# Optimization experiments

Measured on AMD Instinct MI355X. Metric: run time of the kernel, lower is better.

## Reference

```python
import jax, jax.numpy as jnp
import numpy as np

NEG_SLOPE = 0.2


def setup_inputs() -> dict:
    key = jax.random.key(0)
    ks = jax.random.split(key, 12)
    N, D = 50000, 256
    H, C = 4, 128          # heads, per-head channels; H*C = gnn_hidden_dim = 512
    E = 800000
    edge_index = jax.random.randint(ks[0], (2, E), 0, N, dtype=jnp.int64)
    edge_weight = jax.random.uniform(ks[1], (E,), dtype=jnp.float32)
    s = 1.0 / np.sqrt(D)
    return {
        'edge_index': edge_index,
        'edge_weight': edge_weight,
        'emb':     jax.random.normal(ks[2], (N, D), jnp.float32),
        'W':       jax.random.normal(ks[3], (D, H * C), jnp.float32) * s,
        'att_src': jax.random.normal(ks[4], (H, C), jnp.float32) * s,
        'att_dst': jax.random.normal(ks[5], (H, C), jnp.float32) * s,
        'att_edge': jax.random.normal(ks[6], (H, C), jnp.float32) * s,
        'W_edge':  jax.random.normal(ks[7], (1, H * C), jnp.float32),
        'bias':    jnp.zeros((H * C,), jnp.float32),
        'W_out':   jax.random.normal(ks[8], (H * C, D), jnp.float32) * s,
        'b_out':   jnp.zeros((D,), jnp.float32),
    }


def reference(edge_index, edge_weight, emb, W, att_src, att_dst, att_edge,
              W_edge, bias, W_out, b_out):
    N, D = emb.shape
    H, C = att_src.shape
    src, dst = edge_index[0], edge_index[1]
    E = src.shape[0]

    # GATConv: shared linear projection for src and dst (in_channels is int)
    x = (emb @ W).reshape(N, H, C)                     # [N,H,C]

    # add self loops; edge_attr for loops = per-dst mean of incoming edge_attr
    ones = jnp.ones((E,), emb.dtype)
    cnt = jax.ops.segment_sum(ones, dst, num_segments=N)
    ea_mean = jax.ops.segment_sum(edge_weight, dst, num_segments=N) / jnp.maximum(cnt, 1.0)
    loop = jnp.arange(N, dtype=src.dtype)
    src_f = jnp.concatenate([src, loop])
    dst_f = jnp.concatenate([dst, loop])
    ea = jnp.concatenate([edge_weight, ea_mean])[:, None]   # [E+N, 1]

    e_feat = (ea @ W_edge).reshape(-1, H, C)            # [E+N,H,C]

    a_src = jnp.einsum('nhc,hc->nh', x, att_src)        # [N,H]
    a_dst = jnp.einsum('nhc,hc->nh', x, att_dst)
    a_e = jnp.einsum('ehc,hc->eh', e_feat, att_edge)    # [E+N,H]

    alpha = jax.nn.leaky_relu(a_src[src_f] + a_dst[dst_f] + a_e, NEG_SLOPE)
    # segment softmax over destination neighborhoods
    m = jax.ops.segment_max(alpha, dst_f, num_segments=N)
    alpha = jnp.exp(alpha - m[dst_f])
    denom = jax.ops.segment_sum(alpha, dst_f, num_segments=N)
    alpha = alpha / (denom[dst_f] + 1e-16)              # [E+N,H]

    msg = x[src_f] * alpha[..., None]                   # [E+N,H,C]
    out = jax.ops.segment_sum(msg, dst_f, num_segments=N).reshape(N, H * C) + bias

    return out @ W_out + b_out                          # [N,D]
```

## Files before the change

### kernel.cpp

```cpp
#include <hip/hip_runtime.h>
#include <cstdint>
#include <cstddef>

#define NEG_SLOPE 0.2f
#define HC 512
#define NH 4
#define CAP 64

typedef __attribute__((ext_vector_type(8))) short bf16x8;
typedef __attribute__((ext_vector_type(4))) float f32x4;

__device__ inline float lrelu(float z) { return z > 0.f ? z : NEG_SLOPE * z; }

__device__ inline unsigned short f2bf(float f) {
    unsigned u = __float_as_uint(f);
    u += 0x7FFFu + ((u >> 16) & 1u);
    return (unsigned short)(u >> 16);
}
__device__ inline float bflo(unsigned v) { return __uint_as_float(v << 16); }
__device__ inline float bfhi(unsigned v) { return __uint_as_float(v & 0xffff0000u); }

#define GLOAD16(gp, lp) \
    __builtin_amdgcn_global_load_lds( \
        (const __attribute__((address_space(1))) unsigned int*)(const void*)(gp), \
        (__attribute__((address_space(3))) unsigned int*)(void*)(lp), 16, 0, 0)

__global__ __launch_bounds__(256) void mega1_kernel(
        const int* __restrict__ ei, const float* __restrict__ ew, int E,
        int* __restrict__ cnt, int2* __restrict__ csr2,
        const float* __restrict__ W, const float* __restrict__ W_out,
        const float* __restrict__ att_s, const float* __restrict__ att_d,
        const float* __restrict__ W_edge, const float* __restrict__ att_edge,
        const float* __restrict__ bias, const float* __restrict__ b_out,
        unsigned short* __restrict__ Wb, unsigned short* __restrict__ WoT,
        float* __restrict__ watt, float* __restrict__ bc4, float* __restrict__ sh,
        const float4* __restrict__ embf4, uint2* __restrict__ embq,
        int nQuads, int nCast) {
    int b = blockIdx.x, t = threadIdx.x;
    int r6 = b % 6, q6 = b / 6;

    if (r6 == 0) {
        int lane = t & 63;
        unsigned long long nzm = __ballot(ei[2 * lane + 1] != 0);
        int is64 = (nzm == 0ull) ? 1 : 0;
        int base = q6 * 1024;

        int dv[4], sv[4];
        float wv[4];
        bool ok[4];
        #pragma unroll
        for (int r = 0; r < 4; ++r) {
            int e = base + r * 256 + t;
            ok[r] = (e < E);
            if (ok[r]) {
                size_t de = (size_t)E + e;
                dv[r] = is64 ? ei[2 * de] : ei[de];
                sv[r] = is64 ? ei[2 * (size_t)e] : ei[e];
                wv[r] = ew[e];
            }
        }
        int pos[4];
        #pragma unroll
        for (int r = 0; r < 4; ++r)
            if (ok[r]) pos[r] = atomicAdd(&cnt[dv[r]], 1);
        #pragma unroll
        for (int r = 0; r < 4; ++r)
            if (ok[r] && pos[r] < CAP)
                csr2[(size_t)dv[r] * CAP + pos[r]] =
                    make_int2(sv[r], __float_as_int(wv[r]));
        return;
    }

    int aux = q6 * 5 + r6 - 1;
    if (aux < 128) {
        int i = aux * 256 + t;
        float4 v = reinterpret_cast<const float4*>(W)[i];
        ushort4 o;
        o.x = f2bf(v.x); o.y = f2bf(v.y); o.z = f2bf(v.z); o.w = f2bf(v.w);
        reinterpret_cast<ushort4*>(Wb)[i] = o;
    } else if (aux < 640) {
        int idx = (aux - 128) * 256 + t;
        int r = idx >> 8, c = idx & 255;
        WoT[(size_t)c * 512 + r] = f2bf(W_out[idx]);
    } else if (aux < 648) {
        int i = aux - 640;
        int h = i & 3;
        const float* att = (i < 4) ? att_s : att_d;
        float s = 0.f;
        for (int c = 0; c < 128; ++c)
            s += W[(size_t)t * HC + h * 128 + c] * att[h * 128 + c];
        watt[i * 256 + t] = s;
    } else if (aux < 652) {
        int part = aux - 648;
        int j0 = part * 128;
        float s = (part == 0) ? b_out[t] : 0.f;
        for (int j = j0; j < j0 + 128; ++j)
            s += bias[j] * W_out[(size_t)j * 256 + t];
        bc4[part * 256 + t] = s;
    } else if (aux == 652) {
        if (t < NH) {
            float s = 0.f;
            for (int c = 0; c < 128; ++c)
                s += W_edge[t * 128 + c] * att_edge[t * 128 + c];
            sh[t] = s;
        }
    } else if (aux < 653 + nCast) {
        int base = (aux - 653) * 1024;
        #pragma unroll
        for (int j = 0; j < 4; ++j) {
            int i = base + j * 256 + t;
            if (i < nQuads) {
                float4 v = embf4[i];
                uint2 o;
                o.x = (unsigned)f2bf(v.x) | ((unsigned)f2bf(v.y) << 16);
                o.y = (unsigned)f2bf(v.z) | ((unsigned)f2bf(v.w) << 16);
                embq[i] = o;
            }
        }
    }
}

__global__ __launch_bounds__(256) void mega2_kernel(
        const unsigned short* __restrict__ WoT, const unsigned short* __restrict__ Wb,
        unsigned short* __restrict__ MT,
        const uint2* __restrict__ embq, const float* __restrict__ watt,
        float* __restrict__ a_src, float* __restrict__ a_dst, int N) {
    __shared__ __align__(16) char smem[32768];
    int b = blockIdx.x, t = threadIdx.x;

    if (b < 16) {
        unsigned short* As = (unsigned short*)smem;
        unsigned short* Bs = (unsigned short*)(smem + 16384);
        int lane = t & 63, w = t >> 6;
        int bn = (b & 1) * 128, bm = ((b >> 1) & 1) * 128, z = b >> 2;
        const unsigned short* A  = WoT + (size_t)z * 128;
        const unsigned short* BT = Wb  + (size_t)z * 128;
        int wr = w >> 1, wc = w & 1;

        f32x4 acc[4][4];
        #pragma unroll
        for (int i = 0; i < 4; ++i)
            #pragma unroll
            for (int j = 0; j < 4; ++j)
                acc[i][j] = (f32x4){0.f, 0.f, 0.f, 0.f};

        int lr = lane & 15, kb = lane >> 4;
        int q = lane & 7;

        for (int k0 = 0; k0 < 128; k0 += 64) {
            #pragma unroll
            for (int p = 0; p < 4; ++p) {
                int row = p * 32 + w * 8 + (lane >> 3);
                int ce  = ((q ^ (row & 7)) << 3) + k0;
                int ob  = p * 4096 + w * 1024;
                GLOAD16(A  + (size_t)(bm + row) * 512 + ce, (char*)As + ob);
                GLOAD16(BT + (size_t)(bn + row) * 512 + ce, (char*)Bs + ob);
            }
            __syncthreads();
            #pragma unroll
            for (int kk = 0; kk < 2; ++kk) {
                bf16x8 a[4], bfr[4];
                #pragma unroll
                for (int i = 0; i < 4; ++i) {
                    int row = wr * 64 + i * 16 + lr;
                    a[i] = *reinterpret_cast<const bf16x8*>(
                        &As[row * 64 + (((kk * 4 + kb) ^ (row & 7)) << 3)]);
                }
                #pragma unroll
                for (int j = 0; j < 4; ++j) {
                    int row = wc * 64 + j * 16 + lr;
                    bfr[j] = *reinterpret_cast<const bf16x8*>(
                        &Bs[row * 64 + (((kk * 4 + kb) ^ (row & 7)) << 3)]);
                }
                #pragma unroll
                for (int i = 0; i < 4; ++i)
                    #pragma unroll
                    for (int j = 0; j < 4; ++j)
                        acc[i][j] = __builtin_amdgcn_mfma_f32_16x16x32_bf16(a[i], bfr[j], acc[i][j], 0, 0, 0);
            }
            __syncthreads();
        }
        int rg = lane >> 4;
        #pragma unroll
        for (int i = 0; i < 4; ++i)
            #pragma unroll
            for (int r = 0; r < 4; ++r) {
                int row = bm + wr * 64 + i * 16 + rg * 4 + r;
                #pragma unroll
                for (int j = 0; j < 4; ++j) {
                    int col = bn + wc * 64 + j * 16 + lr;
                    MT[(size_t)row * 1024 + z * 256 + col] = f2bf(acc[i][j][r]);
                }
            }
    } else {
        int bb = b - 16;
        int wid = t >> 6, lane = t & 63;
        #pragma unroll
        for (int j = 0; j < 4; ++j) {
            int n = bb * 16 + wid * 4 + j;
            if (n >= N) break;
            uint2 v = embq[(size_t)n * 64 + lane];
            float d0 = bflo(v.x), d1 = bfhi(v.x), d2 = bflo(v.y), d3 = bfhi(v.y);
            float r[8];
            #pragma unroll
            for (int i = 0; i < 8; ++i) {
                float4 wv = reinterpret_cast<const float4*>(watt)[i * 64 + lane];
                r[i] = d0 * wv.x + d1 * wv.y + d2 * wv.z + d3 * wv.w;
            }
            #pragma unroll
            for (int off = 32; off > 0; off >>= 1) {
                #pragma unroll
                for (int i = 0; i < 8; ++i) r[i] += __shfl_xor(r[i], off);
            }
            if (lane == 0) {
                size_t bofs = (size_t)n * 4;
                a_src[bofs + 0] = r[0]; a_src[bofs + 1] = r[1];
                a_src[bofs + 2] = r[2]; a_src[bofs + 3] = r[3];
                a_dst[bofs + 0] = r[4]; a_dst[bofs + 1] = r[5];
                a_dst[bofs + 2] = r[6]; a_dst[bofs + 3] = r[7];
            }
        }
    }
}

#define EFMA(W_, V_) { \
    float e0_ = bflo(V_.x), e1_ = bfhi(V_.x), e2_ = bflo(V_.y), e3_ = bfhi(V_.y); \
    a00 += W_.x * e0_; a01 += W_.x * e1_; a02 += W_.x * e2_; a03 += W_.x * e3_; \
    a10 += W_.y * e0_; a11 += W_.y * e1_; a12 += W_.y * e2_; a13 += W_.y * e3_; \
    a20 += W_.z * e0_; a21 += W_.z * e1_; a22 += W_.z * e2_; a23 += W_.z * e3_; \
    a30 += W_.w * e0_; a31 += W_.w * e1_; a32 += W_.w * e2_; a33 += W_.w * e3_; \
    den0 += W_.x; den1 += W_.y; den2 += W_.z; den3 += W_.w; }

__global__ __launch_bounds__(256) void agg_kernel(
        const uint2* __restrict__ embq, const float* __restrict__ a_src,
        const float* __restrict__ a_dst, const int* __restrict__ cnt,
        const float* __restrict__ sh, const int2* __restrict__ csr2,
        uint2* __restrict__ aggn, int N) {
    int wid = threadIdx.x >> 6, lane = threadIdx.x & 63;
    int n = blockIdx.x * 4 + wid;
    if (n >= N) return;
    int deg = cnt[n];
    int m = deg < CAP ? deg : CAP;

    __shared__ int s_src[4][64];
    __shared__ __align__(16) float s_alpha[4][64][4];

    int k1 = 0x7FFFFFFF, k2 = 0x7FFFFFFF;
    if (lane < m) {
        int2 p = csr2[(size_t)n * CAP + lane];
        k1 = p.x; k2 = p.y;
    }
    #pragma unroll
    for (int k = 2; k <= 64; k <<= 1) {
        #pragma unroll
        for (int j = k >> 1; j > 0; j >>= 1) {
            int o1 = __shfl_xor(k1, j);
            int o2 = __shfl_xor(k2, j);
            bool lower = (lane & j) == 0;
            bool asc = (lane & k) == 0;
            bool cmp = (k1 > o1) || (k1 == o1 && k2 > o2);
            if ((cmp == lower) == asc) { k1 = o1; k2 = o2; }
        }
    }
    float wgt = (lane < m) ? __int_as_float(k2) : 0.f;

    float wsl = wgt;
    #pragma unroll
    for (int o = 32; o > 0; o >>= 1) wsl += __shfl_xor(wsl, o);
    float eam = wsl / fmaxf((float)deg, 1.f);

    float ad0 = a_dst[(size_t)n * 4 + 0], ad1 = a_dst[(size_t)n * 4 + 1];
    float ad2 = a_dst[(size_t)n * 4 + 2], ad3 = a_dst[(size_t)n * 4 + 3];
    float sh0 = sh[0], sh1 = sh[1], sh2 = sh[2], sh3 = sh[3];
    float es0 = __expf(lrelu(a_src[(size_t)n * 4 + 0] + ad0 + eam * sh0));
    float es1 = __expf(lrelu(a_src[(size_t)n * 4 + 1] + ad1 + eam * sh1));
    float es2 = __expf(lrelu(a_src[(size_t)n * 4 + 2] + ad2 + eam * sh2));
    float es3 = __expf(lrelu(a_src[(size_t)n * 4 + 3] + ad3 + eam * sh3));

    uint2 xv = embq[(size_t)n * 64 + lane];
    float d0 = bflo(xv.x), d1 = bfhi(xv.x), d2 = bflo(xv.y), d3 = bfhi(xv.y);

    float a00 = es0 * d0, a01 = es0 * d1, a02 = es0 * d2, a03 = es0 * d3;
    float a10 = es1 * d0, a11 = es1 * d1, a12 = es1 * d2, a13 = es1 * d3;
    float a20 = es2 * d0, a21 = es2 * d1, a22 = es2 * d2, a23 = es2 * d3;
    float a30 = es3 * d0, a31 = es3 * d1, a32 = es3 * d2, a33 = es3 * d3;
    float den0 = es0, den1 = es1, den2 = es2, den3 = es3;

    if (lane < m) {
        int s = k1;
        s_src[wid][lane] = s;
        float4 as4 = *reinterpret_cast<const float4*>(&a_src[(size_t)s * 4]);
        s_alpha[wid][lane][0] = __expf(lrelu(as4.x + ad0 + wgt * sh0));
        s_alpha[wid][lane][1] = __expf(lrelu(as4.y + ad1 + wgt * sh1));
        s_alpha[wid][lane][2] = __expf(lrelu(as4.z + ad2 + wgt * sh2));
        s_alpha[wid][lane][3] = __expf(lrelu(as4.w + ad3 + wgt * sh3));
    }
    int e2 = 0;
    for (; e2 + 2 <= m; e2 += 2) {
        int s0 = s_src[wid][e2], s1 = s_src[wid][e2 + 1];
        float4 w0 = *reinterpret_cast<const float4*>(s_alpha[wid][e2]);
        float4 w1 = *reinterpret_cast<const float4*>(s_alpha[wid][e2 + 1]);
        uint2 v0 = embq[(size_t)s0 * 64 + lane];
        uint2 v1 = embq[(size_t)s1 * 64 + lane];
        EFMA(w0, v0); EFMA(w1, v1);
    }
    if (e2 < m) {
        int s0 = s_src[wid][e2];
        float4 w0 = *reinterpret_cast<const float4*>(s_alpha[wid][e2]);
        uint2 v0 = embq[(size_t)s0 * 64 + lane];
        EFMA(w0, v0);
    }

    float i0 = 1.f / (den0 + 1e-16f), i1 = 1.f / (den1 + 1e-16f);
    float i2 = 1.f / (den2 + 1e-16f), i3 = 1.f / (den3 + 1e-16f);
    size_t base = (size_t)n * 256 + lane;
    uint2 o;
    o.x = (unsigned)f2bf(a00 * i0) | ((unsigned)f2bf(a01 * i0) << 16);
    o.y = (unsigned)f2bf(a02 * i0) | ((unsigned)f2bf(a03 * i0) << 16);
    aggn[base] = o;
    o.x = (unsigned)f2bf(a10 * i1) | ((unsigned)f2bf(a11 * i1) << 16);
    o.y = (unsigned)f2bf(a12 * i1) | ((unsigned)f2bf(a13 * i1) << 16);
    aggn[base + 64] = o;
    o.x = (unsigned)f2bf(a20 * i2) | ((unsigned)f2bf(a21 * i2) << 16);
    o.y = (unsigned)f2bf(a22 * i2) | ((unsigned)f2bf(a23 * i2) << 16);
    aggn[base + 128] = o;
    o.x = (unsigned)f2bf(a30 * i3) | ((unsigned)f2bf(a31 * i3) << 16);
    o.y = (unsigned)f2bf(a32 * i3) | ((unsigned)f2bf(a33 * i3) << 16);
    aggn[base + 192] = o;
}

__global__ __launch_bounds__(512) void gemm_out_kernel(
        const unsigned short* __restrict__ A,
        const unsigned short* __restrict__ BT,
        const float* __restrict__ bc4, float* __restrict__ C, int M) {
    __shared__ __align__(16) unsigned short As[128 * 64];
    __shared__ __align__(16) unsigned short Bs[256 * 64];
    int tid = threadIdx.x;
    int lane = tid & 63, w = tid >> 6;
    int bm = blockIdx.x * 128;
    int wr = w >> 2, wc = w & 3;

    f32x4 acc[4][4];
    #pragma unroll
    for (int i = 0; i < 4; ++i)
        #pragma unroll
        for (int j = 0; j < 4; ++j)
            acc[i][j] = (f32x4){0.f, 0.f, 0.f, 0.f};

    int lr = lane & 15, kb = lane >> 4;
    int q = lane & 7;

    for (int k0 = 0; k0 < 1024; k0 += 64) {
        #pragma unroll
        for (int p = 0; p < 2; ++p) {
            int row = p * 64 + w * 8 + (lane >> 3);
            int ce  = ((q ^ (row & 7)) << 3) + k0;
            int ob  = p * 8192 + w * 1024;
            int gr = bm + row; if (gr >= M) gr = M - 1;
            GLOAD16(A + (size_t)gr * 1024 + ce, (char*)As + ob);
        }
        #pragma unroll
        for (int p = 0; p < 4; ++p) {
            int row = p * 64 + w * 8 + (lane >> 3);
            int ce  = ((q ^ (row & 7)) << 3) + k0;
            int ob  = p * 8192 + w * 1024;
            GLOAD16(BT + (size_t)row * 1024 + ce, (char*)Bs + ob);
        }
        __syncthreads();

        #pragma unroll
        for (int kk = 0; kk < 2; ++kk) {
            bf16x8 a[4], b[4];
            #pragma unroll
            for (int i = 0; i < 4; ++i) {
                int row = wr * 64 + i * 16 + lr;
                a[i] = *reinterpret_cast<const bf16x8*>(
                    &As[row * 64 + (((kk * 4 + kb) ^ (row & 7)) << 3)]);
            }
            #pragma unroll
            for (int j = 0; j < 4; ++j) {
                int row = wc * 64 + j * 16 + lr;
                b[j] = *reinterpret_cast<const bf16x8*>(
                    &Bs[row * 64 + (((kk * 4 + kb) ^ (row & 7)) << 3)]);
            }
            #pragma unroll
            for (int i = 0; i < 4; ++i)
                #pragma unroll
                for (int j = 0; j < 4; ++j)
                    acc[i][j] = __builtin_amdgcn_mfma_f32_16x16x32_bf16(a[i], b[j], acc[i][j], 0, 0, 0);
        }
        __syncthreads();
    }

    int rg = lane >> 4;
    #pragma unroll
    for (int i = 0; i < 4; ++i) {
        #pragma unroll
        for (int r = 0; r < 4; ++r) {
            int row = bm + wr * 64 + i * 16 + rg * 4 + r;
            if (row >= M) continue;
            #pragma unroll
            for (int j = 0; j < 4; ++j) {
                int col = wc * 64 + j * 16 + lr;
                float bval = bc4[col] + bc4[256 + col] + bc4[512 + col] + bc4[768 + col];
                C[(size_t)row * 256 + col] = acc[i][j][r] + bval;
            }
        }
    }
}

extern "C" void kernel_launch(void* const* d_in, const int* in_sizes, int n_in,
                              void* d_out, int out_size, void* d_ws, size_t ws_size,
                              hipStream_t stream) {
    const int*   edge_index  = (const int*)d_in[0];
    const float* edge_weight = (const float*)d_in[1];
    const float* emb         = (const float*)d_in[2];
    const float* W           = (const float*)d_in[3];
    const float* att_src     = (const float*)d_in[4];
    const float* att_dst     = (const float*)d_in[5];
    const float* att_edge    = (const float*)d_in[6];
    const float* W_edge      = (const float*)d_in[7];
    const float* bias        = (const float*)d_in[8];
    const float* W_out       = (const float*)d_in[9];
    const float* b_out       = (const float*)d_in[10];
    float* out = (float*)d_out;

    const int E = in_sizes[1];
    const int D = 256;
    const int N = in_sizes[2] / D;
    const int mb = (N + 127) / 128;
    const int nEmb = (N + 15) / 16;
    const int nEdge4 = (E + 1023) / 1024;
    const int nQuads = N * 64;
    const int nCast = (nQuads + 1023) / 1024;

    char* ws = (char*)d_ws;
    size_t off = 0;
    auto alloc = [&](size_t bytes) {
        size_t o = off;
        off += (bytes + 255) & ~(size_t)255;
        return o;
    };
    unsigned short* embb  = (unsigned short*)(ws + alloc((size_t)N * D * 2));
    unsigned short* aggn  = (unsigned short*)(ws + alloc((size_t)N * 1024 * 2));
    unsigned short* Wb    = (unsigned short*)(ws + alloc((size_t)D * HC * 2));
    unsigned short* WoT   = (unsigned short*)(ws + alloc((size_t)HC * D * 2));
    unsigned short* MT    = (unsigned short*)(ws + alloc((size_t)256 * 1024 * 2));
    float* watt    = (float*)(ws + alloc(2048 * 4));
    float* bc4     = (float*)(ws + alloc(1024 * 4));
    float* a_src   = (float*)(ws + alloc((size_t)N * 4 * 4));
    float* a_dst   = (float*)(ws + alloc((size_t)N * 4 * 4));
    float* sh      = (float*)(ws + alloc(64));
    size_t zbytes  = (size_t)N * 4;
    size_t zoff    = alloc(zbytes);
    int*   cnt     = (int*)(ws + zoff);
    int2*  csr2    = (int2*)(ws + alloc((size_t)N * CAP * 8));
    (void)ws_size; (void)n_in; (void)out_size;

    hipMemsetAsync(ws + zoff, 0, zbytes, stream);

    mega1_kernel<<<nEdge4 * 6, 256, 0, stream>>>(
        edge_index, edge_weight, E, cnt, csr2,
        W, W_out, att_src, att_dst, W_edge, att_edge, bias, b_out,
        Wb, WoT, watt, bc4, sh,
        (const float4*)emb, (uint2*)embb, nQuads, nCast);

    mega2_kernel<<<16 + nEmb, 256, 0, stream>>>(
        WoT, Wb, MT, (const uint2*)embb, watt, a_src, a_dst, N);

    agg_kernel<<<(N + 3) / 4, 256, 0, stream>>>(
        (const uint2*)embb, a_src, a_dst, cnt, sh, csr2, (uint2*)aggn, N);

    gemm_out_kernel<<<mb, 512, 0, stream>>>(aggn, MT, bc4, out, N);
}
```

Baseline: 231.3 us.

## Fuse emb cast with attention-score projection and split small precompute kernel

Measured after the change: 226.0 us, median of 2. 2.3% less time.

```diff
diff --git a/kernel.cpp b/kernel.cpp
--- a/kernel.cpp
+++ b/kernel.cpp
@@ -25,17 +25,49 @@
         (const __attribute__((address_space(1))) unsigned int*)(const void*)(gp), \
         (__attribute__((address_space(3))) unsigned int*)(void*)(lp), 16, 0, 0)
 
+__global__ __launch_bounds__(256) void prep00_kernel(
+        const float* __restrict__ W, const float* __restrict__ W_out,
+        const float* __restrict__ att_s, const float* __restrict__ att_d,
+        const float* __restrict__ W_edge, const float* __restrict__ att_edge,
+        const float* __restrict__ bias, const float* __restrict__ b_out,
+        float* __restrict__ watt, float* __restrict__ bc4, float* __restrict__ sh,
+        uint4* __restrict__ zptr, int zcount) {
+    int b = blockIdx.x, t = threadIdx.x;
+    if (b < 8) {
+        int h = b & 3;
+        const float* att = (b < 4) ? att_s : att_d;
+        float s = 0.f;
+        for (int c = 0; c < 128; ++c)
+            s += W[(size_t)t * HC + h * 128 + c] * att[h * 128 + c];
+        watt[b * 256 + t] = s;
+    } else if (b < 12) {
+        int part = b - 8;
+        int j0 = part * 128;
+        float s = (part == 0) ? b_out[t] : 0.f;
+        for (int j = j0; j < j0 + 128; ++j)
+            s += bias[j] * W_out[(size_t)j * 256 + t];
+        bc4[part * 256 + t] = s;
+    } else if (b == 12) {
+        if (t < NH) {
+            float s = 0.f;
+            for (int c = 0; c < 128; ++c)
+                s += W_edge[t * 128 + c] * att_edge[t * 128 + c];
+            sh[t] = s;
+        }
+    } else {
+        int idx = (b - 13) * 256 + t;
+        if (idx < zcount) zptr[idx] = (uint4){0u, 0u, 0u, 0u};
+    }
+}
+
 __global__ __launch_bounds__(256) void mega1_kernel(
         const int* __restrict__ ei, const float* __restrict__ ew, int E,
         int* __restrict__ cnt, int2* __restrict__ csr2,
         const float* __restrict__ W, const float* __restrict__ W_out,
-        const float* __restrict__ att_s, const float* __restrict__ att_d,
-        const float* __restrict__ W_edge, const float* __restrict__ att_edge,
-        const float* __restrict__ bias, const float* __restrict__ b_out,
         unsigned short* __restrict__ Wb, unsigned short* __restrict__ WoT,
-        float* __restrict__ watt, float* __restrict__ bc4, float* __restrict__ sh,
-        const float4* __restrict__ embf4, uint2* __restrict__ embq,
-        int nQuads, int nCast) {
+        const float4* __restrict__ embf4, const float* __restrict__ watt,
+        uint2* __restrict__ embq, float* __restrict__ a_src,
+        float* __restrict__ a_dst, int N, int nEmb) {
     int b = blockIdx.x, t = threadIdx.x;
     int r6 = b % 6, q6 = b / 6;
 
@@ -82,130 +114,23 @@
         int idx = (aux - 128) * 256 + t;
         int r = idx >> 8, c = idx & 255;
         WoT[(size_t)c * 512 + r] = f2bf(W_out[idx]);
-    } else if (aux < 648) {
-        int i = aux - 640;
-        int h = i & 3;
-        const float* att = (i < 4) ? att_s : att_d;
-        float s = 0.f;
-        for (int c = 0; c < 128; ++c)
-            s += W[(size_t)t * HC + h * 128 + c] * att[h * 128 + c];
-        watt[i * 256 + t] = s;
-    } else if (aux < 652) {
-        int part = aux - 648;
-        int j0 = part * 128;
-        float s = (part == 0) ? b_out[t] : 0.f;
-        for (int j = j0; j < j0 + 128; ++j)
-            s += bias[j] * W_out[(size_t)j * 256 + t];
-        bc4[part * 256 + t] = s;
-    } else if (aux == 652) {
-        if (t < NH) {
-            float s = 0.f;
-            for (int c = 0; c < 128; ++c)
-                s += W_edge[t * 128 + c] * att_edge[t * 128 + c];
-            sh[t] = s;
-        }
-    } else if (aux < 653 + nCast) {
-        int base = (aux - 653) * 1024;
-        #pragma unroll
-        for (int j = 0; j < 4; ++j) {
-            int i = base + j * 256 + t;
-            if (i < nQuads) {
-                float4 v = embf4[i];
-                uint2 o;
-                o.x = (unsigned)f2bf(v.x) | ((unsigned)f2bf(v.y) << 16);
-                o.y = (unsigned)f2bf(v.z) | ((unsigned)f2bf(v.w) << 16);
-                embq[i] = o;
-            }
-        }
-    }
-}
-
-__global__ __launch_bounds__(256) void mega2_kernel(
-        const unsigned short* __restrict__ WoT, const unsigned short* __restrict__ Wb,
-        unsigned short* __restrict__ MT,
-        const uint2* __restrict__ embq, const float* __restrict__ watt,
-        float* __restrict__ a_src, float* __restrict__ a_dst, int N) {
-    __shared__ __align__(16) char smem[32768];
-    int b = blockIdx.x, t = threadIdx.x;
-
-    if (b < 16) {
-        unsigned short* As = (unsigned short*)smem;
-        unsigned short* Bs = (unsigned short*)(smem + 16384);
-        int lane = t & 63, w = t >> 6;
-        int bn = (b & 1) * 128, bm = ((b >> 1) & 1) * 128, z = b >> 2;
-        const unsigned short* A  = WoT + (size_t)z * 128;
-        const unsigned short* BT = Wb  + (size_t)z * 128;
-        int wr = w >> 1, wc = w & 1;
-
-        f32x4 acc[4][4];
-        #pragma unroll
-        for (int i = 0; i < 4; ++i)
-            #pragma unroll
-            for (int j = 0; j < 4; ++j)
-                acc[i][j] = (f32x4){0.f, 0.f, 0.f, 0.f};
-
-        int lr = lane & 15, kb = lane >> 4;
-        int q = lane & 7;
-
-        for (int k0 = 0; k0 < 128; k0 += 64) {
-            #pragma unroll
-            for (int p = 0; p < 4; ++p) {
-                int row = p * 32 + w * 8 + (lane >> 3);
-                int ce  = ((q ^ (row & 7)) << 3) + k0;
-                int ob  = p * 4096 + w * 1024;
-                GLOAD16(A  + (size_t)(bm + row) * 512 + ce, (char*)As + ob);
-                GLOAD16(BT + (size_t)(bn + row) * 512 + ce, (char*)Bs + ob);
-            }
-            __syncthreads();
-            #pragma unroll
-            for (int kk = 0; kk < 2; ++kk) {
-                bf16x8 a[4], bfr[4];
-                #pragma unroll
-                for (int i = 0; i < 4; ++i) {
-                    int row = wr * 64 + i * 16 + lr;
-                    a[i] = *reinterpret_cast<const bf16x8*>(
-                        &As[row * 64 + (((kk * 4 + kb) ^ (row & 7)) << 3)]);
-                }
-                #pragma unroll
-                for (int j = 0; j < 4; ++j) {
-                    int row = wc * 64 + j * 16 + lr;
-                    bfr[j] = *reinterpret_cast<const bf16x8*>(
-                        &Bs[row * 64 + (((kk * 4 + kb) ^ (row & 7)) << 3)]);
-                }
-                #pragma unroll
-                for (int i = 0; i < 4; ++i)
-                    #pragma unroll
-                    for (int j = 0; j < 4; ++j)
-                        acc[i][j] = __builtin_amdgcn_mfma_f32_16x16x32_bf16(a[i], bfr[j], acc[i][j], 0, 0, 0);
-            }
-            __syncthreads();
-        }
-        int rg = lane >> 4;
-        #pragma unroll
-        for (int i = 0; i < 4; ++i)
-            #pragma unroll
-            for (int r = 0; r < 4; ++r) {
-                int row = bm + wr * 64 + i * 16 + rg * 4 + r;
-                #pragma unroll
-                for (int j = 0; j < 4; ++j) {
-                    int col = bn + wc * 64 + j * 16 + lr;
-                    MT[(size_t)row * 1024 + z * 256 + col] = f2bf(acc[i][j][r]);
-                }
-            }
-    } else {
-        int bb = b - 16;
+    } else if (aux < 640 + nEmb) {
+        int bb = aux - 640;
         int wid = t >> 6, lane = t & 63;
         #pragma unroll
         for (int j = 0; j < 4; ++j) {
             int n = bb * 16 + wid * 4 + j;
             if (n >= N) break;
-            uint2 v = embq[(size_t)n * 64 + lane];
-            float d0 = bflo(v.x), d1 = bfhi(v.x), d2 = bflo(v.y), d3 = bfhi(v.y);
+            float4 v = embf4[(size_t)n * 64 + lane];
+            uint2 o;
+            o.x = (unsigned)f2bf(v.x) | ((unsigned)f2bf(v.y) << 16);
+            o.y = (unsigned)f2bf(v.z) | ((unsigned)f2bf(v.w) << 16);
+            embq[(size_t)n * 64 + lane] = o;
             float r[8];
             #pragma unroll
             for (int i = 0; i < 8; ++i) {
                 float4 wv = reinterpret_cast<const float4*>(watt)[i * 64 + lane];
-                r[i] = d0 * wv.x + d1 * wv.y + d2 * wv.z + d3 * wv.w;
+                r[i] = v.x * wv.x + v.y * wv.y + v.z * wv.z + v.w * wv.w;
             }
             #pragma unroll
             for (int off = 32; off > 0; off >>= 1) {
@@ -221,6 +146,75 @@
             }
         }
     }
+}
+
+__global__ __launch_bounds__(256) void mt_kernel(
+        const unsigned short* __restrict__ WoT, const unsigned short* __restrict__ Wb,
+        unsigned short* __restrict__ MT) {
+    __shared__ __align__(16) unsigned short As[128 * 64];
+    __shared__ __align__(16) unsigned short Bs[128 * 64];
+    int b = blockIdx.x, t = threadIdx.x;
+    int lane = t & 63, w = t >> 6;
+    int bn = (b & 1) * 128, bm = ((b >> 1) & 1) * 128, z = b >> 2;
+    const unsigned short* A  = WoT + (size_t)z * 128;
+    const unsigned short* BT = Wb  + (size_t)z * 128;
+    int wr = w >> 1, wc = w & 1;
+
+    f32x4 acc[4][4];
+    #pragma unroll
+    for (int i = 0; i < 4; ++i)
+        #pragma unroll
+        for (int j = 0; j < 4; ++j)
+            acc[i][j] = (f32x4){0.f, 0.f, 0.f, 0.f};
+
+    int lr = lane & 15, kb = lane >> 4;
+    int q = lane & 7;
+
+    for (int k0 = 0; k0 < 128; k0 += 64) {
+        #pragma unroll
+        for (int p = 0; p < 4; ++p) {
+            int row = p * 32 + w * 8 + (lane >> 3);
+            int ce  = ((q ^ (row & 7)) << 3) + k0;
+            int ob  = p * 4096 + w * 1024;
+            GLOAD16(A  + (size_t)(bm + row) * 512 + ce, (char*)As + ob);
+            GLOAD16(BT + (size_t)(bn + row) * 512 + ce, (char*)Bs + ob);
+        }
+        __syncthreads();
+        #pragma unroll
+        for (int kk = 0; kk < 2; ++kk) {
+            bf16x8 a[4], bfr[4];
+            #pragma unroll
+            for (int i = 0; i < 4; ++i) {
+                int row = wr * 64 + i * 16 + lr;
+                a[i] = *reinterpret_cast<const bf16x8*>(
+                    &As[row * 64 + (((kk * 4 + kb) ^ (row & 7)) << 3)]);
+            }
+            #pragma unroll
+            for (int j = 0; j < 4; ++j) {
+                int row = wc * 64 + j * 16 + lr;
+                bfr[j] = *reinterpret_cast<const bf16x8*>(
+                    &Bs[row * 64 + (((kk * 4 + kb) ^ (row & 7)) << 3)]);
+            }
+            #pragma unroll
+            for (int i = 0; i < 4; ++i)
+                #pragma unroll
+                for (int j = 0; j < 4; ++j)
+                    acc[i][j] = __builtin_amdgcn_mfma_f32_16x16x32_bf16(a[i], bfr[j], acc[i][j], 0, 0, 0);
+        }
+        __syncthreads();
+    }
+    int rg = lane >> 4;
+    #pragma unroll
+    for (int i = 0; i < 4; ++i)
+        #pragma unroll
+        for (int r = 0; r < 4; ++r) {
+            int row = bm + wr * 64 + i * 16 + rg * 4 + r;
+            #pragma unroll
+            for (int j = 0; j < 4; ++j) {
+                int col = bn + wc * 64 + j * 16 + lr;
+                MT[(size_t)row * 1024 + z * 256 + col] = f2bf(acc[i][j][r]);
+            }
+        }
 }
 
 #define EFMA(W_, V_) { \
@@ -431,8 +425,6 @@
     const int mb = (N + 127) / 128;
     const int nEmb = (N + 15) / 16;
     const int nEdge4 = (E + 1023) / 1024;
-    const int nQuads = N * 64;
-    const int nCast = (nQuads + 1023) / 1024;
 
     char* ws = (char*)d_ws;
     size_t off = 0;
@@ -451,22 +443,25 @@
     float* a_src   = (float*)(ws + alloc((size_t)N * 4 * 4));
     float* a_dst   = (float*)(ws + alloc((size_t)N * 4 * 4));
     float* sh      = (float*)(ws + alloc(64));
-    size_t zbytes  = (size_t)N * 4;
+    size_t zbytes  = ((size_t)N * 4 + 15) & ~(size_t)15;
     size_t zoff    = alloc(zbytes);
     int*   cnt     = (int*)(ws + zoff);
     int2*  csr2    = (int2*)(ws + alloc((size_t)N * CAP * 8));
     (void)ws_size; (void)n_in; (void)out_size;
 
-    hipMemsetAsync(ws + zoff, 0, zbytes, stream);
+    int zcount = (int)(zbytes / 16);
+    int nz = (zcount + 255) / 256;
+
+    prep00_kernel<<<13 + nz, 256, 0, stream>>>(
+        W, W_out, att_src, att_dst, W_edge, att_edge, bias, b_out,
+        watt, bc4, sh, (uint4*)(ws + zoff), zcount);
 
     mega1_kernel<<<nEdge4 * 6, 256, 0, stream>>>(
         edge_index, edge_weight, E, cnt, csr2,
-        W, W_out, att_src, att_dst, W_edge, att_edge, bias, b_out,
-        Wb, WoT, watt, bc4, sh,
-        (const float4*)emb, (uint2*)embb, nQuads, nCast);
-
-    mega2_kernel<<<16 + nEmb, 256, 0, stream>>>(
-        WoT, Wb, MT, (const uint2*)embb, watt, a_src, a_dst, N);
+        W, W_out, Wb, WoT,
+        (const float4*)emb, watt, (uint2*)embb, a_src, a_dst, N, nEmb);
+
+    mt_kernel<<<16, 256, 0, stream>>>(WoT, Wb, MT);
 
     agg_kernel<<<(N + 3) / 4, 256, 0, stream>>>(
         (const uint2*)embb, a_src, a_dst, cnt, sh, csr2, (uint2*)aggn, N);
```
